# Performance work log

Hardware: AMD Instinct MI355X
Metric: run time of the kernel (lower is better)

## Reference

```python
import jax, jax.numpy as jnp
import numpy as np

EMBED_DIM = 1024
NUM_HEADS = 16
HEAD_DIM = EMBED_DIM // NUM_HEADS
B, N = 2, 2048
BIAS_S = 32


def _interp_matrix(n, s):
    # Bilinear interpolation (align_corners=True) along one axis as an (n, s) matrix.
    pos = jnp.arange(n, dtype=jnp.float32) * ((s - 1) / (n - 1))
    i0 = jnp.floor(pos).astype(jnp.int32)
    i1 = jnp.minimum(i0 + 1, s - 1)
    frac = pos - i0.astype(jnp.float32)
    rows = jnp.arange(n)
    M = jnp.zeros((n, s), dtype=jnp.float32)
    M = M.at[rows, i0].add(1.0 - frac).at[rows, i1].add(frac)
    return M


def setup_inputs() -> dict:
    key = jax.random.key(0)
    ks = jax.random.split(key, 12)
    std = 0.02
    d = {
        'x': jax.random.normal(ks[0], (B, N, EMBED_DIM), dtype=jnp.float32),
        'Wq': jax.random.normal(ks[1], (EMBED_DIM, EMBED_DIM), dtype=jnp.float32) * std,
        'bq': jnp.zeros((EMBED_DIM,), dtype=jnp.float32),
        'Wk': jax.random.normal(ks[2], (EMBED_DIM, EMBED_DIM), dtype=jnp.float32) * std,
        'bk': jnp.zeros((EMBED_DIM,), dtype=jnp.float32),
        'Wv': jax.random.normal(ks[3], (EMBED_DIM, EMBED_DIM), dtype=jnp.float32) * std,
        'bv': jnp.zeros((EMBED_DIM,), dtype=jnp.float32),
        'Wo': jax.random.normal(ks[4], (EMBED_DIM, EMBED_DIM), dtype=jnp.float32) * std,
        'bo': jnp.zeros((EMBED_DIM,), dtype=jnp.float32),
        'gamma': jnp.ones((EMBED_DIM,), dtype=jnp.float32),
        'beta': jnp.zeros((EMBED_DIM,), dtype=jnp.float32),
        'rel_bias': jax.random.normal(ks[5], (NUM_HEADS, BIAS_S, BIAS_S), dtype=jnp.float32) * std,
    }
    return d


def reference(x, Wq, bq, Wk, bk, Wv, bv, Wo, bo, gamma, beta, rel_bias):
    Bx, Nx, C = x.shape
    H, D = NUM_HEADS, HEAD_DIM
    scale = 1.0 / jnp.sqrt(jnp.float32(D))

    # LayerNorm
    mu = jnp.mean(x, axis=-1, keepdims=True)
    var = jnp.mean(jnp.square(x - mu), axis=-1, keepdims=True)
    xn = (x - mu) * jax.lax.rsqrt(var + 1e-5) * gamma + beta

    q = (xn @ Wq.T + bq).reshape(Bx, Nx, H, D).transpose(0, 2, 1, 3)
    k = (xn @ Wk.T + bk).reshape(Bx, Nx, H, D).transpose(0, 2, 1, 3)
    v = (xn @ Wv.T + bv).reshape(Bx, Nx, H, D).transpose(0, 2, 1, 3)

    attn = jnp.einsum('bhnd,bhmd->bhnm', q, k) * scale  # [B,H,N,N]

    # Bilinear interp of rel_pos_bias (H,32,32) -> (H,N,N), align_corners=True
    M = _interp_matrix(Nx, BIAS_S)  # (N, 32)
    rel = jnp.einsum('ni,hij,mj->hnm', M, rel_bias, M)
    rel = rel.at[:, -1, :].set(0.0).at[:, :, -1].set(0.0)
    attn = attn + rel[None]

    mask = jnp.triu(jnp.ones((Nx, Nx), dtype=bool), k=1)
    attn = jnp.where(mask, -jnp.inf, attn)
    attn = jax.nn.softmax(attn, axis=-1)

    out = jnp.einsum('bhnm,bhmd->bhnd', attn, v)
    out = out.transpose(0, 2, 1, 3).reshape(Bx, Nx, C)
    out = out @ Wo.T + bo  # dropout is identity in eval mode
    return out
```

## Files before the change

kernel.cpp:

```cpp
#include <hip/hip_runtime.h>
#include <hip/hip_bf16.h>

#define EMBED 1024
#define NHEADS 16
#define HDIM 64
#define NB 2
#define NSEQ 2048
#define NTOK (NB*NSEQ)

using short8  = __attribute__((ext_vector_type(8))) short;
using short4v = __attribute__((ext_vector_type(4))) short;
using f32x4   = __attribute__((ext_vector_type(4))) float;

#define INV_LN2 1.4426950408889634f

__device__ __forceinline__ short f2bf(float x) {
  __hip_bfloat16 h = __float2bfloat16(x);
  short s;
  __builtin_memcpy(&s, &h, 2);
  return s;
}

#define GLDS16(gp, lp) __builtin_amdgcn_global_load_lds( \
    (const __attribute__((address_space(1))) unsigned int*)(const void*)(gp), \
    (__attribute__((address_space(3))) unsigned int*)(void*)(lp), 16, 0, 0)

__global__ __launch_bounds__(256) void ln_kernel(const float* __restrict__ x,
    const float* __restrict__ gamma, const float* __restrict__ beta,
    short* __restrict__ xn) {
  const int row = blockIdx.x;
  const int tid = threadIdx.x;
  const float* xr = x + (size_t)row * EMBED;
  float4 v = *(const float4*)(xr + tid * 4);
  float s  = v.x + v.y + v.z + v.w;
  float s2 = v.x*v.x + v.y*v.y + v.z*v.z + v.w*v.w;
#pragma unroll
  for (int off = 32; off; off >>= 1) {
    s  += __shfl_down(s, off);
    s2 += __shfl_down(s2, off);
  }
  __shared__ float red[8];
  const int wv = tid >> 6, ln = tid & 63;
  if (ln == 0) { red[wv] = s; red[4 + wv] = s2; }
  __syncthreads();
  s  = red[0] + red[1] + red[2] + red[3];
  s2 = red[4] + red[5] + red[6] + red[7];
  const float mu  = s * (1.0f / EMBED);
  const float var = s2 * (1.0f / EMBED) - mu * mu;
  const float inv = rsqrtf(var + 1e-5f);
  float4 g  = *(const float4*)(gamma + tid * 4);
  float4 bt = *(const float4*)(beta + tid * 4);
  short4v o;
  o[0] = f2bf((v.x - mu) * inv * g.x + bt.x);
  o[1] = f2bf((v.y - mu) * inv * g.y + bt.y);
  o[2] = f2bf((v.z - mu) * inv * g.z + bt.z);
  o[3] = f2bf((v.w - mu) * inv * g.w + bt.w);
  *(short4v*)(xn + (size_t)row * EMBED + tid * 4) = o;
}

__global__ __launch_bounds__(256) void cast4_kernel(
    const float* __restrict__ a, const float* __restrict__ b,
    const float* __restrict__ c, const float* __restrict__ d,
    short* __restrict__ oa, short* __restrict__ ob,
    short* __restrict__ oc, short* __restrict__ od) {
  const int wsel = blockIdx.y;
  const float* s = (wsel == 0) ? a : (wsel == 1) ? b : (wsel == 2) ? c : d;
  short* o       = (wsel == 0) ? oa : (wsel == 1) ? ob : (wsel == 2) ? oc : od;
  const int i = (blockIdx.x * 256 + threadIdx.x) * 4;
  float4 v = *(const float4*)(s + i);
  short4v r;
  r[0] = f2bf(v.x); r[1] = f2bf(v.y); r[2] = f2bf(v.z); r[3] = f2bf(v.w);
  *(short4v*)(o + i) = r;
}

template<bool F32OUT>
__global__ __launch_bounds__(256) void gemm_kernel(
    const short* __restrict__ A,
    const short* __restrict__ W0, const short* __restrict__ W1, const short* __restrict__ W2,
    const float* __restrict__ b0, const float* __restrict__ b1, const float* __restrict__ b2,
    void* __restrict__ O0, void* __restrict__ O1, void* __restrict__ O2) {
  constexpr int K = 1024, NOUT = 1024;
  const int z = blockIdx.z;
  const short* Bw   = (z == 0) ? W0 : (z == 1) ? W1 : W2;
  const float* bias = (z == 0) ? b0 : (z == 1) ? b1 : b2;
  void* Cout        = (z == 0) ? O0 : (z == 1) ? O1 : O2;

  const int tn = blockIdx.x, tm = blockIdx.y;
  const int tid = threadIdx.x, w = tid >> 6, lane = tid & 63;
  const int wm = w >> 1, wn = w & 1;
  const int g = lane >> 4, c = lane & 15;

  __shared__ short As[128 * 32];
  __shared__ short Bs[128 * 32];

  f32x4 acc[4][4];
#pragma unroll
  for (int i = 0; i < 4; i++)
#pragma unroll
    for (int j = 0; j < 4; j++) acc[i][j] = (f32x4){0.f, 0.f, 0.f, 0.f};

  const int crow = tid >> 2;
  const int ckc  = tid & 3;
  const short* ga = A  + (size_t)(tm * 128 + crow) * K + ckc * 8;
  const short* gb = Bw + (size_t)(tn * 128 + crow) * K + ckc * 8;
  short* la = &As[tid * 8];
  short* lb = &Bs[tid * 8];

  for (int k0 = 0; k0 < K; k0 += 32) {
    __syncthreads();
    GLDS16(ga + k0, la);
    GLDS16(ga + k0 + (size_t)64 * K, la + 64 * 32);
    GLDS16(gb + k0, lb);
    GLDS16(gb + k0 + (size_t)64 * K, lb + 64 * 32);
    __syncthreads();
    short8 af[4], bfr[4];
#pragma unroll
    for (int mi = 0; mi < 4; mi++)
      af[mi] = *(const short8*)&As[(wm * 64 + mi * 16 + c) * 32 + g * 8];
#pragma unroll
    for (int ni = 0; ni < 4; ni++)
      bfr[ni] = *(const short8*)&Bs[(wn * 64 + ni * 16 + c) * 32 + g * 8];
#pragma unroll
    for (int mi = 0; mi < 4; mi++)
#pragma unroll
      for (int ni = 0; ni < 4; ni++)
        acc[mi][ni] = __builtin_amdgcn_mfma_f32_16x16x32_bf16(af[mi], bfr[ni], acc[mi][ni], 0, 0, 0);
  }

#pragma unroll
  for (int ni = 0; ni < 4; ni++) {
    const int col = tn * 128 + wn * 64 + ni * 16 + c;
    const float bs = bias[col];
#pragma unroll
    for (int mi = 0; mi < 4; mi++) {
#pragma unroll
      for (int j = 0; j < 4; j++) {
        const int row = tm * 128 + wm * 64 + mi * 16 + g * 4 + j;
        const float v = acc[mi][ni][j] + bs;
        if constexpr (F32OUT)
          ((float*)Cout)[(size_t)row * NOUT + col] = v;
        else
          ((short*)Cout)[(size_t)row * NOUT + col] = f2bf(v);
      }
    }
  }
}

__global__ __launch_bounds__(256) void vtrans_kernel(const short* __restrict__ vb,
                                                     short* __restrict__ vt) {
  const int n0 = blockIdx.x * 64;
  const int bh = blockIdx.y;
  const int b = bh >> 4, h = bh & 15;
  const int tid = threadIdx.x;
  __shared__ short tl[64 * 68];

  const int r  = tid >> 3;
  const int c8 = (tid & 7) * 8;
#pragma unroll
  for (int i = 0; i < 2; i++) {
    const int row = r + i * 32;
    short8 v = *(const short8*)(vb + (size_t)(b * NSEQ + n0 + row) * EMBED + h * 64 + c8);
    *(short8*)&tl[row * 68 + c8] = v;
  }
  __syncthreads();
  const int d  = tid >> 2;
  const int ns = (tid & 3) * 16;
  short8 o0, o1;
#pragma unroll
  for (int e = 0; e < 8; e++) {
    o0[e] = tl[(ns + e) * 68 + d];
    o1[e] = tl[(ns + 8 + e) * 68 + d];
  }
  short* dst = vt + ((size_t)((b * 16 + h) * 64 + d)) * 2048 + n0 + ns;
  *(short8*)dst = o0;
  *(short8*)(dst + 8) = o1;
}

__global__ __launch_bounds__(512, 4) void attn_kernel(
    const short* __restrict__ Qm, const short* __restrict__ Km, const short* __restrict__ Vt,
    const float* __restrict__ relb, short* __restrict__ ctx) {
  const int bid = blockIdx.x;
  const int bh  = bid & 31;
  const int idx = bid >> 5;
  const int qpair = (idx < 8) ? (15 - idx) : (idx - 8);
  const int b = bh >> 4, h = bh & 15;
  const int tid = threadIdx.x, w = tid >> 6, lane = tid & 63;
  const int g = lane >> 4, c = lane & 15;
  constexpr float S31 = 31.0f / 2047.0f;

  __shared__ short k_lds[2][64 * 64];
  __shared__ short vt_lds[2][64 * 64];
  __shared__ short p_lds[8][16 * 64];
  __shared__ float rrow[128][33];

  const int qbase = qpair * 128;
  const size_t bhq = (size_t)b * NSEQ * EMBED + h * HDIM;
  const short* vtb = Vt + (size_t)((b << 4) + h) * 64 * 2048;

  short8 qf[2];
  {
    const short* qp = Qm + bhq + (size_t)(qbase + w * 16 + c) * EMBED;
    qf[0] = *(const short8*)(qp + g * 8);
    qf[1] = *(const short8*)(qp + 32 + g * 8);
  }

  const int srow = tid >> 3;
  const int sd0  = (tid & 7) * 8;
  const int swz  = (srow & 7) << 3;

  GLDS16(Km + bhq + (size_t)srow * EMBED + (sd0 ^ swz), &k_lds[0][srow * 64 + sd0]);
  GLDS16(vtb + (size_t)srow * 2048 + (sd0 ^ swz),       &vt_lds[0][srow * 64 + sd0]);
  for (int i = tid; i < 128 * 32; i += 512) {
    const int qr = i >> 5, jj = i & 31;
    const int qg0 = qbase + qr;
    float rv = 0.f;
    if (qg0 != NSEQ - 1) {
      const float pos = qg0 * S31;
      const int i0 = (int)pos;
      const int i1 = min(i0 + 1, 31);
      const float fr = pos - (float)i0;
      const float* T = relb + h * 1024;
      rv = ((1.f - fr) * T[i0 * 32 + jj] + fr * T[i1 * 32 + jj]) * INV_LN2;
    }
    rrow[qr][jj] = rv;
  }
  __syncthreads();

  float mrow = -3.0e38f, lrow = 0.f;
  f32x4 oacc[4];
#pragma unroll
  for (int db = 0; db < 4; db++) oacc[db] = (f32x4){0.f, 0.f, 0.f, 0.f};

  const int qg  = qbase + w * 16 + c;
  const int qhi = qbase + w * 16 + 15;
  const float* rr = &rrow[w * 16 + c][0];
  const int csw = (c & 7) << 3;
  const int nkv = 2 * qpair + 2;

  for (int kt = 0; kt < nkv; kt++) {
    const int cur = kt & 1;
    const int kv0 = kt * 64;

    if (kt + 1 < nkv) {
      GLDS16(Km + bhq + (size_t)(kv0 + 64 + srow) * EMBED + (sd0 ^ swz),
             &k_lds[cur ^ 1][srow * 64 + sd0]);
      GLDS16(vtb + (size_t)srow * 2048 + (kv0 + 64) + (sd0 ^ swz),
             &vt_lds[cur ^ 1][srow * 64 + sd0]);
    }

    if (kv0 <= qhi) {
      const short* kl = &k_lds[cur][0];
      const short* vl = &vt_lds[cur][0];

      f32x4 st[4];
#pragma unroll
      for (int mb = 0; mb < 4; mb++) st[mb] = (f32x4){0.f, 0.f, 0.f, 0.f};
      __builtin_amdgcn_s_setprio(1);
#pragma unroll
      for (int kh = 0; kh < 2; kh++) {
        const int dk = kh * 32 + g * 8;
#pragma unroll
        for (int mb = 0; mb < 4; mb++) {
          const int row = mb * 16 + c;
          short8 kf = *(const short8*)&kl[row * 64 + (dk ^ ((row & 7) << 3))];
          st[mb] = __builtin_amdgcn_mfma_f32_16x16x32_bf16(kf, qf[kh], st[mb], 0, 0, 0);
        }
      }
      __builtin_amdgcn_s_setprio(0);

      float p[4][4];
      float pmax = -3.0e38f;
      const bool diag = (kv0 + 63 > qg);
      const int I = (int)(kv0 * S31);
      const float rA = rr[I];
      const float rB = rr[I + 1];
      const float rC = rr[min(I + 2, 31)];
      const float dAB = rB - rA, dBC = rC - rB;
#pragma unroll
      for (int mb = 0; mb < 4; mb++) {
#pragma unroll
        for (int j = 0; j < 4; j++) {
          const int mg = kv0 + mb * 16 + g * 4 + j;
          const float pos = mg * S31;
          const int i0 = (int)pos;
          const float fr = pos - (float)i0;
          const bool sel = i0 > I;
          float sv = st[mb][j] * (0.125f * INV_LN2);
          if (mg != NSEQ - 1) sv += fmaf(fr, sel ? dBC : dAB, sel ? rB : rA);
          if (diag && mg > qg) sv = -3.0e38f;
          p[mb][j] = sv;
          pmax = fmaxf(pmax, sv);
        }
      }
      pmax = fmaxf(pmax, __shfl_xor(pmax, 16));
      pmax = fmaxf(pmax, __shfl_xor(pmax, 32));

      if (!__all(pmax - mrow <= 11.6f)) {
        const float mnew = fmaxf(mrow, pmax);
        const float al = exp2f(mrow - mnew);
        mrow = mnew;
        lrow *= al;
        float alj[4];
#pragma unroll
        for (int j = 0; j < 4; j++) alj[j] = __shfl(al, g * 4 + j);
#pragma unroll
        for (int db = 0; db < 4; db++)
#pragma unroll
          for (int j = 0; j < 4; j++) oacc[db][j] *= alj[j];
      }

      float rs = 0.f;
#pragma unroll
      for (int mb = 0; mb < 4; mb++)
#pragma unroll
        for (int j = 0; j < 4; j++) {
          const float pe = exp2f(p[mb][j] - mrow);
          p[mb][j] = pe;
          rs += pe;
        }
      rs += __shfl_xor(rs, 16);
      rs += __shfl_xor(rs, 32);
      lrow += rs;

      short* pw = &p_lds[w][0];
#pragma unroll
      for (int mb = 0; mb < 4; mb++)
#pragma unroll
        for (int jh = 0; jh < 2; jh++) {
          const int m = mb * 16 + g * 4 + jh * 2;
          unsigned int pk = ((unsigned int)(unsigned short)f2bf(p[mb][jh * 2 + 1]) << 16)
                          |  (unsigned int)(unsigned short)f2bf(p[mb][jh * 2]);
          *(unsigned int*)&pw[c * 64 + (m ^ csw)] = pk;
        }

      __builtin_amdgcn_s_setprio(1);
#pragma unroll
      for (int kb = 0; kb < 2; kb++) {
        const int m0 = kb * 32 + g * 8;
        short8 pa = *(const short8*)&pw[c * 64 + (m0 ^ csw)];
#pragma unroll
        for (int db = 0; db < 4; db++) {
          const int d = db * 16 + c;
          short8 vf = *(const short8*)&vl[d * 64 + (m0 ^ ((d & 7) << 3))];
          oacc[db] = __builtin_amdgcn_mfma_f32_16x16x32_bf16(pa, vf, oacc[db], 0, 0, 0);
        }
      }
      __builtin_amdgcn_s_setprio(0);
    }
    __syncthreads();
  }

  float linv[4];
#pragma unroll
  for (int j = 0; j < 4; j++) linv[j] = 1.f / __shfl(lrow, g * 4 + j);
#pragma unroll
  for (int j = 0; j < 4; j++) {
    short* op = ctx + bhq + (size_t)(qbase + w * 16 + g * 4 + j) * EMBED;
#pragma unroll
    for (int db = 0; db < 4; db++)
      op[db * 16 + c] = f2bf(oacc[db][j] * linv[j]);
  }
}

extern "C" void kernel_launch(void* const* d_in, const int* in_sizes, int n_in,
                              void* d_out, int out_size, void* d_ws, size_t ws_size,
                              hipStream_t stream) {
  const float* x     = (const float*)d_in[0];
  const float* Wq    = (const float*)d_in[1];
  const float* bq    = (const float*)d_in[2];
  const float* Wk    = (const float*)d_in[3];
  const float* bk    = (const float*)d_in[4];
  const float* Wv    = (const float*)d_in[5];
  const float* bv    = (const float*)d_in[6];
  const float* Wo    = (const float*)d_in[7];
  const float* bo    = (const float*)d_in[8];
  const float* gamma = (const float*)d_in[9];
  const float* beta  = (const float*)d_in[10];
  const float* relb  = (const float*)d_in[11];
  float* out = (float*)d_out;

  char* ws = (char*)d_ws;
  short* xn  = (short*)ws; ws += (size_t)NTOK * EMBED * 2;
  short* wqb = (short*)ws; ws += (size_t)EMBED * EMBED * 2;
  short* wkb = (short*)ws; ws += (size_t)EMBED * EMBED * 2;
  short* wvb = (short*)ws; ws += (size_t)EMBED * EMBED * 2;
  short* wob = (short*)ws; ws += (size_t)EMBED * EMBED * 2;
  short* qb  = (short*)ws; ws += (size_t)NTOK * EMBED * 2;
  short* kb_ = (short*)ws; ws += (size_t)NTOK * EMBED * 2;
  short* vb  = (short*)ws; ws += (size_t)NTOK * EMBED * 2;
  short* ctx = (short*)ws; ws += (size_t)NTOK * EMBED * 2;
  short* vtb = xn;

  ln_kernel<<<dim3(NTOK), dim3(256), 0, stream>>>(x, gamma, beta, xn);
  cast4_kernel<<<dim3(1024, 4), dim3(256), 0, stream>>>(Wq, Wk, Wv, Wo, wqb, wkb, wvb, wob);
  gemm_kernel<false><<<dim3(8, 32, 3), dim3(256), 0, stream>>>(
      xn, wqb, wkb, wvb, bq, bk, bv, (void*)qb, (void*)kb_, (void*)vb);
  vtrans_kernel<<<dim3(32, 32), dim3(256), 0, stream>>>(vb, vtb);
  attn_kernel<<<dim3(512), dim3(512), 0, stream>>>(qb, kb_, vtb, relb, ctx);
  gemm_kernel<true><<<dim3(8, 32, 1), dim3(256), 0, stream>>>(
      ctx, wob, wob, wob, bo, bo, bo, (void*)out, (void*)out, (void*)out);
}
```

Before: 234.8 us.

## Replace QKV projection GEMM with 256x256-tile double-buffered pipelined kernel

```diff
diff --git a/kernel.cpp b/kernel.cpp
--- a/kernel.cpp
+++ b/kernel.cpp
@@ -24,6 +24,9 @@
 #define GLDS16(gp, lp) __builtin_amdgcn_global_load_lds( \
     (const __attribute__((address_space(1))) unsigned int*)(const void*)(gp), \
     (__attribute__((address_space(3))) unsigned int*)(void*)(lp), 16, 0, 0)
+
+#define BAR() __builtin_amdgcn_s_barrier()
+#define WAITVM(N) asm volatile("s_waitcnt vmcnt(" #N ")" ::: "memory")
 
 __global__ __launch_bounds__(256) void ln_kernel(const float* __restrict__ x,
     const float* __restrict__ gamma, const float* __restrict__ beta,
@@ -73,6 +76,143 @@
   *(short4v*)(o + i) = r;
 }
 
+__global__ __launch_bounds__(512, 2) void qkv_kernel(
+    const short* __restrict__ A,
+    const short* __restrict__ W0, const short* __restrict__ W1, const short* __restrict__ W2,
+    const float* __restrict__ b0, const float* __restrict__ b1, const float* __restrict__ b2,
+    short* __restrict__ O0, short* __restrict__ O1, short* __restrict__ O2) {
+  constexpr int K = 1024, kNT = 16;
+  const int tn = blockIdx.x, tm = blockIdx.y;
+  const int sel = tn >> 2;
+  const short* Bw   = (sel == 0) ? W0 : (sel == 1) ? W1 : W2;
+  const float* bias = (sel == 0) ? b0 : (sel == 1) ? b1 : b2;
+  short* Cout       = (sel == 0) ? O0 : (sel == 1) ? O1 : O2;
+  const int ncol0 = (tn & 3) * 256;
+
+  const int tid = threadIdx.x;
+  const int w = tid >> 6, lane = tid & 63;
+  const int wr = w >> 2, wc = w & 3;
+  const int g = lane >> 4, c = lane & 15;
+
+  __shared__ short As[2][256 * 64];
+  __shared__ short Bs[2][256 * 64];
+
+  f32x4 acc[8][4];
+#pragma unroll
+  for (int i = 0; i < 8; i++)
+#pragma unroll
+    for (int j = 0; j < 4; j++) acc[i][j] = (f32x4){0.f, 0.f, 0.f, 0.f};
+
+  const int sr  = tid >> 3;
+  const int sc8 = (tid & 7) * 8;
+  const int ssw = (sr & 7) << 3;
+  const short* ga = A  + (size_t)(tm * 256) * K;
+  const short* gb = Bw + (size_t)ncol0 * K;
+
+  auto stA = [&](int buf, int unit, int kt) {
+#pragma unroll
+    for (int i = 0; i < 2; i++) {
+      const int row = unit * 64 + i * 128 + sr;
+      GLDS16(ga + (size_t)row * K + kt * 64 + (sc8 ^ ssw), &As[buf][row * 64 + sc8]);
+    }
+  };
+  auto stB = [&](int buf, int unit, int kt) {
+#pragma unroll
+    for (int i = 0; i < 2; i++) {
+      const int row = unit * 128 + i * 64 + sr;
+      GLDS16(gb + (size_t)row * K + kt * 64 + (sc8 ^ ssw), &Bs[buf][row * 64 + sc8]);
+    }
+  };
+
+  short8 af[4][2], bf[4][2];
+
+  auto ldA = [&](const short* as, int mh) {
+#pragma unroll
+    for (int mi = 0; mi < 4; mi++) {
+      const int row = wr * 128 + mh * 64 + mi * 16 + c;
+      const int sw = (row & 7) << 3;
+#pragma unroll
+      for (int ks = 0; ks < 2; ks++)
+        af[mi][ks] = *(const short8*)&as[row * 64 + ((ks * 32 + g * 8) ^ sw)];
+    }
+  };
+  auto MF = [&](int mh, int nh) {
+#pragma unroll
+    for (int ks = 0; ks < 2; ks++)
+#pragma unroll
+      for (int mi = 0; mi < 4; mi++)
+#pragma unroll
+        for (int ni = 0; ni < 2; ni++)
+          acc[mh * 4 + mi][nh * 2 + ni] = __builtin_amdgcn_mfma_f32_16x16x32_bf16(
+              af[mi][ks], bf[nh * 2 + ni][ks], acc[mh * 4 + mi][nh * 2 + ni], 0, 0, 0);
+  };
+
+  stA(0, 0, 0); stA(0, 1, 0); stB(0, 0, 0); stB(0, 1, 0);
+  stA(1, 0, 1); stA(1, 1, 1); stB(1, 0, 1); stB(1, 1, 1);
+  WAITVM(8);
+  BAR();
+
+  for (int kt = 0; kt < kNT; ++kt) {
+    const int cb = kt & 1;
+    const short* as = As[cb];
+    const short* bs = Bs[cb];
+    const bool pre = (kt + 2 < kNT);
+
+    ldA(as, 0);
+#pragma unroll
+    for (int ni = 0; ni < 4; ni++) {
+      const int row = wc * 64 + ni * 16 + c;
+      const int sw = (row & 7) << 3;
+#pragma unroll
+      for (int ks = 0; ks < 2; ks++)
+        bf[ni][ks] = *(const short8*)&bs[row * 64 + ((ks * 32 + g * 8) ^ sw)];
+    }
+    BAR();
+    __builtin_amdgcn_s_setprio(1);
+    MF(0, 0);
+    __builtin_amdgcn_s_setprio(0);
+    BAR();
+
+    if (pre) stA(cb, 0, kt + 2);
+    BAR();
+    __builtin_amdgcn_s_setprio(1);
+    MF(0, 1);
+    __builtin_amdgcn_s_setprio(0);
+    BAR();
+
+    ldA(as, 1);
+    if (pre) stB(cb, 0, kt + 2);
+    BAR();
+    __builtin_amdgcn_s_setprio(1);
+    MF(1, 0);
+    __builtin_amdgcn_s_setprio(0);
+    BAR();
+
+    if (pre) { stA(cb, 1, kt + 2); stB(cb, 1, kt + 2); }
+    BAR();
+    __builtin_amdgcn_s_setprio(1);
+    MF(1, 1);
+    __builtin_amdgcn_s_setprio(0);
+    if (pre) { WAITVM(8); } else if (kt + 1 < kNT) { WAITVM(0); }
+    BAR();
+  }
+
+#pragma unroll
+  for (int ni4 = 0; ni4 < 4; ni4++) {
+    const int no = (ni4 >> 1) * 32 + (ni4 & 1) * 16;
+    const int lcol = ncol0 + wc * 64 + no + c;
+    const float bsv = bias[lcol];
+#pragma unroll
+    for (int mi8 = 0; mi8 < 8; mi8++) {
+      const int mo = (mi8 >> 2) * 64 + (mi8 & 3) * 16;
+      const int row = tm * 256 + wr * 128 + mo + g * 4;
+#pragma unroll
+      for (int j = 0; j < 4; j++)
+        Cout[(size_t)(row + j) * 1024 + lcol] = f2bf(acc[mi8][ni4][j] + bsv);
+    }
+  }
+}
+
 template<bool F32OUT>
 __global__ __launch_bounds__(256) void gemm_kernel(
     const short* __restrict__ A,
@@ -393,8 +533,8 @@
 
   ln_kernel<<<dim3(NTOK), dim3(256), 0, stream>>>(x, gamma, beta, xn);
   cast4_kernel<<<dim3(1024, 4), dim3(256), 0, stream>>>(Wq, Wk, Wv, Wo, wqb, wkb, wvb, wob);
-  gemm_kernel<false><<<dim3(8, 32, 3), dim3(256), 0, stream>>>(
-      xn, wqb, wkb, wvb, bq, bk, bv, (void*)qb, (void*)kb_, (void*)vb);
+  qkv_kernel<<<dim3(12, 16), dim3(512), 0, stream>>>(
+      xn, wqb, wkb, wvb, bq, bk, bv, qb, kb_, vb);
   vtrans_kernel<<<dim3(32, 32), dim3(256), 0, stream>>>(vb, vtb);
   attn_kernel<<<dim3(512), dim3(512), 0, stream>>>(qb, kb_, vtb, relb, ctx);
   gemm_kernel<true><<<dim3(8, 32, 1), dim3(256), 0, stream>>>(
```

Result: slower. 241.5 us (+2.8%).

## Fold bilinear relative-position bias into the QK MFMA as an extra rank-32 product

Applied to the files above, without the earlier changes.

```diff
diff --git a/kernel.cpp b/kernel.cpp
--- a/kernel.cpp
+++ b/kernel.cpp
@@ -187,11 +187,13 @@
   const int tid = threadIdx.x, w = tid >> 6, lane = tid & 63;
   const int g = lane >> 4, c = lane & 15;
   constexpr float S31 = 31.0f / 2047.0f;
+  constexpr float CSC = 0.125f * INV_LN2;
 
   __shared__ short k_lds[2][64 * 64];
   __shared__ short vt_lds[2][64 * 64];
   __shared__ short p_lds[8][16 * 64];
-  __shared__ float rrow[128][33];
+  __shared__ short rbf[128 * 32];
+  __shared__ short u_lds[2][64 * 40];
 
   const int qbase = qpair * 128;
   const size_t bhq = (size_t)b * NSEQ * EMBED + h * HDIM;
@@ -207,6 +209,24 @@
   const int srow = tid >> 3;
   const int sd0  = (tid & 7) * 8;
   const int swz  = (srow & 7) << 3;
+
+  auto buildU = [&](int buf, int kv) {
+    if (tid < 64) {
+      short* ur = &u_lds[buf][tid * 40];
+      *(int4*)&ur[0]  = (int4){0, 0, 0, 0};
+      *(int4*)&ur[8]  = (int4){0, 0, 0, 0};
+      *(int4*)&ur[16] = (int4){0, 0, 0, 0};
+      *(int4*)&ur[24] = (int4){0, 0, 0, 0};
+      const int m = kv + tid;
+      if (m != NSEQ - 1) {
+        const float pos = m * S31;
+        const int i0 = (int)pos;
+        const float fr = pos - (float)i0;
+        ur[i0]     = f2bf(1.0f - fr);
+        ur[i0 + 1] = f2bf(fr);
+      }
+    }
+  };
 
   GLDS16(Km + bhq + (size_t)srow * EMBED + (sd0 ^ swz), &k_lds[0][srow * 64 + sd0]);
   GLDS16(vtb + (size_t)srow * 2048 + (sd0 ^ swz),       &vt_lds[0][srow * 64 + sd0]);
@@ -220,11 +240,14 @@
       const int i1 = min(i0 + 1, 31);
       const float fr = pos - (float)i0;
       const float* T = relb + h * 1024;
-      rv = ((1.f - fr) * T[i0 * 32 + jj] + fr * T[i1 * 32 + jj]) * INV_LN2;
+      rv = ((1.f - fr) * T[i0 * 32 + jj] + fr * T[i1 * 32 + jj]) * 8.0f;
     }
-    rrow[qr][jj] = rv;
-  }
+    rbf[i] = f2bf(rv);
+  }
+  buildU(0, 0);
   __syncthreads();
+
+  const short8 rq = *(const short8*)&rbf[(w * 16 + c) * 32 + g * 8];
 
   float mrow = -3.0e38f, lrow = 0.f;
   f32x4 oacc[4];
@@ -233,7 +256,6 @@
 
   const int qg  = qbase + w * 16 + c;
   const int qhi = qbase + w * 16 + 15;
-  const float* rr = &rrow[w * 16 + c][0];
   const int csw = (c & 7) << 3;
   const int nkv = 2 * qpair + 2;
 
@@ -246,11 +268,13 @@
              &k_lds[cur ^ 1][srow * 64 + sd0]);
       GLDS16(vtb + (size_t)srow * 2048 + (kv0 + 64) + (sd0 ^ swz),
              &vt_lds[cur ^ 1][srow * 64 + sd0]);
+      buildU(cur ^ 1, kv0 + 64);
     }
 
     if (kv0 <= qhi) {
       const short* kl = &k_lds[cur][0];
       const short* vl = &vt_lds[cur][0];
+      const short* ul = &u_lds[cur][0];
 
       f32x4 st[4];
 #pragma unroll
@@ -266,32 +290,29 @@
           st[mb] = __builtin_amdgcn_mfma_f32_16x16x32_bf16(kf, qf[kh], st[mb], 0, 0, 0);
         }
       }
+#pragma unroll
+      for (int mb = 0; mb < 4; mb++) {
+        short8 uf = *(const short8*)&ul[(mb * 16 + c) * 40 + g * 8];
+        st[mb] = __builtin_amdgcn_mfma_f32_16x16x32_bf16(uf, rq, st[mb], 0, 0, 0);
+      }
       __builtin_amdgcn_s_setprio(0);
 
-      float p[4][4];
-      float pmax = -3.0e38f;
       const bool diag = (kv0 + 63 > qg);
-      const int I = (int)(kv0 * S31);
-      const float rA = rr[I];
-      const float rB = rr[I + 1];
-      const float rC = rr[min(I + 2, 31)];
-      const float dAB = rB - rA, dBC = rC - rB;
-#pragma unroll
-      for (int mb = 0; mb < 4; mb++) {
-#pragma unroll
-        for (int j = 0; j < 4; j++) {
-          const int mg = kv0 + mb * 16 + g * 4 + j;
-          const float pos = mg * S31;
-          const int i0 = (int)pos;
-          const float fr = pos - (float)i0;
-          const bool sel = i0 > I;
-          float sv = st[mb][j] * (0.125f * INV_LN2);
-          if (mg != NSEQ - 1) sv += fmaf(fr, sel ? dBC : dAB, sel ? rB : rA);
-          if (diag && mg > qg) sv = -3.0e38f;
-          p[mb][j] = sv;
-          pmax = fmaxf(pmax, sv);
-        }
-      }
+      if (diag) {
+#pragma unroll
+        for (int mb = 0; mb < 4; mb++)
+#pragma unroll
+          for (int j = 0; j < 4; j++) {
+            const int mg = kv0 + mb * 16 + g * 4 + j;
+            if (mg > qg) st[mb][j] = -1.0e38f;
+          }
+      }
+      float pmr = -3.0e38f;
+#pragma unroll
+      for (int mb = 0; mb < 4; mb++)
+#pragma unroll
+        for (int j = 0; j < 4; j++) pmr = fmaxf(pmr, st[mb][j]);
+      float pmax = pmr * CSC;
       pmax = fmaxf(pmax, __shfl_xor(pmax, 16));
       pmax = fmaxf(pmax, __shfl_xor(pmax, 32));
 
@@ -309,12 +330,13 @@
           for (int j = 0; j < 4; j++) oacc[db][j] *= alj[j];
       }
 
+      float p[4][4];
       float rs = 0.f;
 #pragma unroll
       for (int mb = 0; mb < 4; mb++)
 #pragma unroll
         for (int j = 0; j < 4; j++) {
-          const float pe = exp2f(p[mb][j] - mrow);
+          const float pe = exp2f(fmaf(st[mb][j], CSC, -mrow));
           p[mb][j] = pe;
           rs += pe;
         }
```

After: 217.7 us. -7.3%, faster.
